# Performance work log

Measured on AMD Instinct MI355X. Metric: run time of the kernel, lower is better.

## Reference

```python
import math
import jax, jax.numpy as jnp
import numpy as np

PE_DIM = 128
NUM_HEADS = 8
U = V = 2
TEMP = 10000.0


def sine_pe(y_embed, x_embed, num_pos_feats, temperature, card):
    """Matches get_sine_position_encoding with use_norm=True."""
    eps = 1e-6
    scale = 2.0 * math.pi
    y = y_embed / (card[0] + eps) * scale
    x = x_embed / (card[1] + eps) * scale
    dim_t = jnp.asarray(temperature, jnp.float32) ** (
        2.0 * (jnp.arange(num_pos_feats, dtype=jnp.float32) // 2) / num_pos_feats)
    px = x[..., None] / dim_t
    py = y[..., None] / dim_t

    def interleave(p):
        s = jnp.sin(p[..., 0::2])
        c = jnp.cos(p[..., 1::2])
        return jnp.stack((s, c), axis=-1).reshape(p.shape[:-1] + (-1,))

    return jnp.concatenate((interleave(py), interleave(px)), axis=-1)


def setup_inputs() -> dict:
    key = jax.random.key(0)
    ks = jax.random.split(key, 8)
    B, C, H, W = 2, 64, 256, 256
    dim = C
    # xavier-ish scale for Linear(128 -> 64)
    w_std = math.sqrt(2.0 / (PE_DIM + dim))
    return {
        "feat_supp": jax.random.normal(ks[0], (B, C, H, W), jnp.float32),
        "flow": jax.random.normal(ks[1], (B, H, W, 2), jnp.float32) * 3.0,
        "feat_curr": jax.random.normal(ks[2], (B, C, H, W), jnp.float32),
        "q_w": jax.random.normal(ks[3], (dim, PE_DIM), jnp.float32) * w_std,
        "q_b": jnp.zeros((dim,), jnp.float32),
        "k_w": jax.random.normal(ks[4], (dim, PE_DIM), jnp.float32) * w_std,
        "k_b": jnp.zeros((dim,), jnp.float32),
        "v_w": jax.random.normal(ks[5], (dim, PE_DIM), jnp.float32) * w_std,
        "v_b": jnp.zeros((dim,), jnp.float32),
    }


def reference(feat_supp, flow, feat_curr, q_w, q_b, k_w, k_b, v_w, v_b):
    B, C, H, W = feat_curr.shape
    UV = U * V
    HW = H * W
    nh = NUM_HEADS
    hd = C // nh
    d = PE_DIM // C  # pe channels per feature channel
    scale = hd ** (-0.5)

    # flow-displaced integer grid + fractional part
    img_off = jnp.stack(
        jnp.meshgrid(jnp.arange(H), jnp.arange(W), indexing="ij"), axis=-1
    ).astype(flow.dtype)                                   # (H, W, 2) in (y, x)
    grid_full = img_off[None] + flow[..., ::-1]            # flow flipped to (y, x)
    grid_intg = jnp.floor(grid_full).astype(jnp.int32)
    grid_deci = grid_full - grid_intg                      # (B, H, W, 2)

    win_off = jnp.stack(
        jnp.meshgrid(jnp.arange(U), jnp.arange(V), indexing="ij"), axis=-1
    ).astype(jnp.int32)                                    # (U, V, 2)
    grid_w = grid_intg[:, :, :, None, None, :] + win_off[None, None, None]
    grid_w = grid_w.reshape(B, HW * UV, 2)
    deci = grid_deci.reshape(B, HW, 2)

    # duplicate-padding gather of support features
    h_idx = jnp.clip(grid_w[..., 0], 0, H - 1)
    w_idx = jnp.clip(grid_w[..., 1], 0, W - 1)
    lin = h_idx * W + w_idx                                # (B, HW*UV)
    feat_warp = jnp.take_along_axis(
        feat_supp.reshape(B, C, HW), lin[:, None, :], axis=2)  # (B, C, HW*UV)
    feat_warp = feat_warp.transpose(0, 2, 1).reshape(B, HW, UV, C)

    # window position bias (card = window_size - 1, use_corrected_card=False)
    wy, wx = jnp.meshgrid(jnp.arange(U, dtype=jnp.float32),
                          jnp.arange(V, dtype=jnp.float32), indexing="ij")
    pos_bias = sine_pe(wy.reshape(1, -1), wx.reshape(1, -1),
                       PE_DIM // 2, TEMP, (U - 1, V - 1))   # (1, UV, PE_DIM)
    pe_warp = pos_bias.reshape(1, 1, UV, C, d)
    fw = (feat_warp[..., None] + pe_warp).reshape(B, HW, UV, PE_DIM)

    # current-frame features + fractional-offset positional encoding
    fc = feat_curr.reshape(B, C, HW).transpose(0, 2, 1)     # (B, HW, C)
    pe_curr = sine_pe(deci[..., 0], deci[..., 1],
                      PE_DIM // 2, TEMP, (U, V))            # (B, HW, PE_DIM)
    fc = (fc[..., None] + pe_curr.reshape(B, HW, C, d)).reshape(B, HW, PE_DIM)

    q = (fc @ q_w.T + q_b).reshape(B, HW, nh, hd)
    k = (fw @ k_w.T + k_b).reshape(B, HW, UV, nh, hd)
    v = (fw @ v_w.T + v_b).reshape(B, HW, UV, nh, hd)

    attn = jnp.einsum("bnhd,bnuhd->bnhu", q * scale, k)
    attn = jax.nn.softmax(attn, axis=-1)
    out = jnp.einsum("bnhu,bnuhd->bnhd", attn, v).reshape(B, HW, C)
    return out.reshape(B, H, W, C).transpose(0, 3, 1, 2)
```

## Files before the change

### kernel.cpp

```cpp
#include <hip/hip_runtime.h>
#include <hip/hip_bf16.h>

#define HWHW 65536
#define LN1E4_32 0.28782313662425572f
#define TWO_PI_N 6.2831847f

typedef __attribute__((ext_vector_type(8))) short short8;
typedef __attribute__((ext_vector_type(4))) short s16x4;
typedef __attribute__((ext_vector_type(4))) float f32x4;


__device__ __forceinline__ short f2bf(float f) {
  union { __hip_bfloat16 h; short s; } u;
  u.h = __float2bfloat16(f);
  return u.s;
}

__global__ __launch_bounds__(256)
void pre_pass(const float* __restrict__ supp,
              const float* __restrict__ qw, const float* __restrict__ kw,
              const float* __restrict__ vw,
              const float* __restrict__ kb, const float* __restrict__ vb,
              __hip_bfloat16* __restrict__ suppT,
              __hip_bfloat16* __restrict__ wfrag, float* __restrict__ bias) {
  const int t = threadIdx.x;
  if (blockIdx.x < 2048) {
    __shared__ short tile[64 * 68];
    const int b   = blockIdx.x >> 10;
    const int p0  = (blockIdx.x & 1023) << 6;
    const int px4 = (t & 15) << 2;
    const int g   = t >> 4;

    const float* src = supp + ((size_t)b * 64 + g * 4) * HWHW + p0 + px4;
    f32x4 v[4];
#pragma unroll
    for (int c = 0; c < 4; ++c)
      v[c] = *(const f32x4*)(src + (size_t)c * HWHW);
#pragma unroll
    for (int j = 0; j < 4; ++j) {
      s16x4 pk;
#pragma unroll
      for (int c = 0; c < 4; ++c) pk[c] = f2bf(v[c][j]);
      *(s16x4*)&tile[(px4 + j) * 68 + g * 4] = pk;
    }
    __syncthreads();
    const int px = t >> 2, ch0 = (t & 3) << 4;
    s16x4 r0 = *(s16x4*)&tile[px * 68 + ch0];
    s16x4 r1 = *(s16x4*)&tile[px * 68 + ch0 + 4];
    s16x4 r2 = *(s16x4*)&tile[px * 68 + ch0 + 8];
    s16x4 r3 = *(s16x4*)&tile[px * 68 + ch0 + 12];
    short8 o0, o1;
#pragma unroll
    for (int j = 0; j < 4; ++j) {
      o0[j] = r0[j]; o0[j + 4] = r1[j];
      o1[j] = r2[j]; o1[j + 4] = r3[j];
    }
    short8* dst = (short8*)(suppT + ((size_t)(b * HWHW + p0 + px)) * 64 + ch0);
    dst[0] = o0;
    dst[1] = o1;
  } else if (blockIdx.x < 2056) {
    int slot = (blockIdx.x - 2048) * 256 + t;
    __hip_bfloat16* dst = wfrag + slot * 8;
    if (slot < 1024) {
      int ksnt = slot >> 6, lane = slot & 63;
      int ks = ksnt >> 2, nt = ksnt & 3;
      const float* w = qw + (nt * 16 + (lane & 15)) * 128 + ks * 32 + (lane >> 4) * 8;
#pragma unroll
      for (int j = 0; j < 8; ++j) dst[j] = __float2bfloat16(w[j]);
    } else {
      int mat = (slot >= 1536);
      int rem = slot & 511;
      int ksnt = rem >> 6, lane = rem & 63;
      int ks = ksnt >> 2, nt = ksnt & 3;
      int c0 = ks * 32 + (lane >> 4) * 8;
      const float* w = (mat ? vw : kw) + (nt * 16 + (lane & 15)) * 128;
#pragma unroll
      for (int j = 0; j < 8; ++j)
        dst[j] = __float2bfloat16(w[2 * (c0 + j)] + w[2 * (c0 + j) + 1]);
    }
  } else {
    for (int s = t; s < 512; s += 256) {
      int mat = s >> 8, uv = (s >> 6) & 3, c = s & 63;
      const float* w = (mat ? vw : kw) + c * 128;
      float acc = (mat ? vb : kb)[c];
      for (int kk = 0; kk < 128; ++kk) {
        float val = (kk < 64 ? (float)(uv >> 1) : (float)(uv & 1)) * TWO_PI_N;
        int i = kk & 63, f = i >> 1;
        float arg = val * __expf(-(float)f * LN1E4_32);
        float pe = (i & 1) ? __cosf(arg) : __sinf(arg);
        acc += pe * w[kk];
      }
      bias[s] = acc;
    }
  }
}

__global__ __attribute__((amdgpu_waves_per_eu(4, 4))) __launch_bounds__(256)
void iw_main(const __hip_bfloat16* __restrict__ suppT, const float* __restrict__ flow,
             const float* __restrict__ feat_curr,
             const short8* __restrict__ wg, const float* __restrict__ bias_g,
             const float* __restrict__ q_b, float* __restrict__ out)
{
  __shared__ __align__(16) char smem[35072];
  short8* lds_kv   = (short8*)smem;
  f32x4*  lds_bias = (f32x4*)(smem + 16384);
  short8* lds_qw   = (short8*)(smem + 18432);
  float*  outstage = (float*)(smem + 18432);

  const int tid = threadIdx.x;
  const int idx = ((blockIdx.x & 7) << 8) | (blockIdx.x >> 3);
  const int b   = idx >> 10;
  const int hw0 = (idx & 1023) << 6;
  const int lane = tid & 63, wv = tid >> 6;
  const int quad = lane >> 4, l15 = lane & 15;
  const int uvl  = l15 & 3;
  const int prow = l15 >> 2;
  const short8* sT = (const short8*)suppT;

#pragma unroll
  for (int j = 0; j < 4; ++j) {
    lds_qw[j * 256 + tid] = wg[j * 256 + tid];
    lds_kv[j * 256 + tid] = wg[1024 + j * 256 + tid];
  }
  {
    float* bl = (float*)lds_bias;
#pragma unroll
    for (int s_ = 0; s_ < 2; ++s_) {
      int s = s_ * 256 + tid;
      int mat = s >> 8, rem = s & 255, r = rem >> 6, c = rem & 63;
      bl[mat * 256 + (c >> 4) * 64 + (c & 15) * 4 + r] = bias_g[s];
    }
  }
  __syncthreads();

  float invd[2][4];
#pragma unroll
  for (int a = 0; a < 2; ++a)
#pragma unroll
    for (int jj = 0; jj < 4; ++jj)
      invd[a][jj] = __expf(-(float)(a * 16 + quad * 4 + jj) * LN1E4_32);

  int iy, ix;
  f32x4 qacc[4];

  {
    const int qpix = hw0 + wv * 16 + l15;
    float2 fl = ((const float2*)flow)[b * HWHW + qpix];
    float gy = (float)(qpix >> 8) + fl.y;
    float gx = (float)(qpix & 255) + fl.x;
    float fy = floorf(gy), fx = floorf(gx);
    iy = (int)fy; ix = (int)fx;
    float vy = (gy - fy) * (6.2831853071795864f / 2.000001f);
    float vx = (gx - fx) * (6.2831853071795864f / 2.000001f);

    short8 qa[4];
#pragma unroll
    for (int ks = 0; ks < 4; ++ks) {
      float val = (ks < 2) ? vy : vx;
#pragma unroll
      for (int jj = 0; jj < 4; ++jj) {
        int c = ks * 16 + quad * 4 + jj;
        float feat = feat_curr[(b * 64 + c) * HWHW + qpix];
        float arg = val * invd[ks & 1][jj];
        qa[ks][jj * 2]     = f2bf(feat + __sinf(arg));
        qa[ks][jj * 2 + 1] = f2bf(feat + __cosf(arg));
      }
    }
#pragma unroll
    for (int nt = 0; nt < 4; ++nt) qacc[nt] = (f32x4){0.f, 0.f, 0.f, 0.f};
#pragma unroll
    for (int ks = 0; ks < 4; ++ks)
#pragma unroll
      for (int nt = 0; nt < 4; ++nt)
        qacc[nt] = __builtin_amdgcn_mfma_f32_16x16x32_bf16(
            qa[ks], lds_qw[(ks * 4 + nt) * 64 + lane], qacc[nt], 0, 0, 0);
  }

  int off[4];
#pragma unroll
  for (int m = 0; m < 4; ++m) {
    int p  = m * 4 + prow;
    int yy = min(max(__shfl(iy, p) + (uvl >> 1), 0), 255);
    int xx = min(max(__shfl(ix, p) + (uvl & 1), 0), 255);
    off[m] = (b * HWHW + yy * 256 + xx) * 8;
  }

  __syncthreads();

  short8 ka[4][2];
#pragma unroll
  for (int m = 0; m < 4; ++m) {
    ka[m][0] = sT[off[m] + quad];
    ka[m][1] = sT[off[m] + 4 + quad];
  }

  float qT[4][4];
  {
#pragma unroll
    for (int nt = 0; nt < 4; ++nt) {
      float qb = q_b[nt * 16 + l15];
#pragma unroll
      for (int r = 0; r < 4; ++r)
        qacc[nt][r] = (qacc[nt][r] + qb) * 0.35355339059327373f;
    }
#pragma unroll
    for (int mt = 0; mt < 4; ++mt)
#pragma unroll
      for (int nt = 0; nt < 4; ++nt) {
        int src = mt * 16 + l15;
        float v0 = __shfl(qacc[nt][0], src);
        float v1 = __shfl(qacc[nt][1], src);
        float v2 = __shfl(qacc[nt][2], src);
        float v3 = __shfl(qacc[nt][3], src);
        float t0 = (quad & 2) ? v2 : v0;
        float t1 = (quad & 2) ? v3 : v1;
        qT[mt][nt] = (quad & 1) ? t1 : t0;
      }
  }

#pragma unroll
  for (int nt = 0; nt < 4; ++nt) {
    short8 kf0 = lds_kv[nt * 64 + lane];
    short8 kf1 = lds_kv[(4 + nt) * 64 + lane];
    short8 vf0 = lds_kv[(8 + nt) * 64 + lane];
    short8 vf1 = lds_kv[(12 + nt) * 64 + lane];
    f32x4 kb4 = lds_bias[nt * 16 + l15];
    f32x4 vb4 = lds_bias[64 + nt * 16 + l15];

#pragma unroll
    for (int mt = 0; mt < 4; ++mt) {
      f32x4 kacc = kb4;
      f32x4 vacc = vb4;
      kacc = __builtin_amdgcn_mfma_f32_16x16x32_bf16(ka[mt][0], kf0, kacc, 0, 0, 0);
      kacc = __builtin_amdgcn_mfma_f32_16x16x32_bf16(ka[mt][1], kf1, kacc, 0, 0, 0);
      vacc = __builtin_amdgcn_mfma_f32_16x16x32_bf16(ka[mt][0], vf0, vacc, 0, 0, 0);
      vacc = __builtin_amdgcn_mfma_f32_16x16x32_bf16(ka[mt][1], vf1, vacc, 0, 0, 0);

      float lg[4];
#pragma unroll
      for (int r = 0; r < 4; ++r) {
        float p = qT[mt][nt] * kacc[r];
        p += __shfl_xor(p, 1);
        p += __shfl_xor(p, 2);
        p += __shfl_xor(p, 4);
        lg[r] = p;
      }
      float mx = fmaxf(fmaxf(lg[0], lg[1]), fmaxf(lg[2], lg[3]));
      float e0 = __expf(lg[0] - mx), e1 = __expf(lg[1] - mx);
      float e2 = __expf(lg[2] - mx), e3 = __expf(lg[3] - mx);
      float inv = 1.0f / (e0 + e1 + e2 + e3);
      float o = (e0 * vacc[0] + e1 * vacc[1] + e2 * vacc[2] + e3 * vacc[3]) * inv;
      outstage[(nt * 16 + l15) * 65 + wv * 16 + mt * 4 + quad] = o;
    }
  }

  __syncthreads();
#pragma unroll
  for (int i = 0; i < 16; ++i) {
    int j = i * 256 + tid;
    int c = j >> 6, p = j & 63;
    out[(b * 64 + c) * HWHW + hw0 + p] = outstage[c * 65 + p];
  }
}

extern "C" void kernel_launch(void* const* d_in, const int* in_sizes, int n_in,
                              void* d_out, int out_size, void* d_ws, size_t ws_size,
                              hipStream_t stream) {
  const float* feat_supp = (const float*)d_in[0];
  const float* flow      = (const float*)d_in[1];
  const float* feat_curr = (const float*)d_in[2];
  const float* q_w = (const float*)d_in[3];
  const float* q_b = (const float*)d_in[4];
  const float* k_w = (const float*)d_in[5];
  const float* k_b = (const float*)d_in[6];
  const float* v_w = (const float*)d_in[7];
  const float* v_b = (const float*)d_in[8];
  float* out = (float*)d_out;
  (void)in_sizes; (void)n_in; (void)out_size; (void)ws_size;

  __hip_bfloat16* wfrag = (__hip_bfloat16*)d_ws;
  float* bias           = (float*)((char*)d_ws + 32768);
  __hip_bfloat16* suppT = (__hip_bfloat16*)((char*)d_ws + 65536);

  hipLaunchKernelGGL(pre_pass, dim3(2057), dim3(256), 0, stream,
                     feat_supp, q_w, k_w, v_w, k_b, v_b, suppT, wfrag, bias);
  hipLaunchKernelGGL(iw_main, dim3(2048), dim3(256), 0, stream,
                     suppT, flow, feat_curr, (const short8*)d_ws, bias, q_b, out);
}
```

Baseline: 153.1 us.

## Read weights from global instead of LDS, raise occupancy, use DPP reductions

The per-block copy of the Q/K/V weight fragments into shared memory is removed. The fragments are now read straight from global memory, with a double-buffered register prefetch for the Q projection. This shrinks LDS from about 35 KB to about 18.7 KB, drops one block barrier, and relaxes the waves-per-EU hint from 4 to 5–8 so more blocks can be resident to hide gather latency. The three shuffle-xor reductions are replaced with DPP quad-perm and half-mirror moves. In exchange, every wave issues repeated cached global loads for the weights, and the tighter register budget could cause spills.

Result: slower. 159.2 us (+4.0%).

```diff
diff --git a/kernel.cpp b/kernel.cpp
--- a/kernel.cpp
+++ b/kernel.cpp
@@ -95,17 +95,15 @@
   }
 }
 
-__global__ __attribute__((amdgpu_waves_per_eu(4, 4))) __launch_bounds__(256)
+__global__ __attribute__((amdgpu_waves_per_eu(5, 8))) __launch_bounds__(256)
 void iw_main(const __hip_bfloat16* __restrict__ suppT, const float* __restrict__ flow,
              const float* __restrict__ feat_curr,
              const short8* __restrict__ wg, const float* __restrict__ bias_g,
              const float* __restrict__ q_b, float* __restrict__ out)
 {
-  __shared__ __align__(16) char smem[35072];
-  short8* lds_kv   = (short8*)smem;
-  f32x4*  lds_bias = (f32x4*)(smem + 16384);
-  short8* lds_qw   = (short8*)(smem + 18432);
-  float*  outstage = (float*)(smem + 18432);
+  __shared__ __align__(16) char smem[18688];
+  f32x4* lds_bias = (f32x4*)smem;
+  float* outstage = (float*)(smem + 2048);
 
   const int tid = threadIdx.x;
   const int idx = ((blockIdx.x & 7) << 8) | (blockIdx.x >> 3);
@@ -117,11 +115,6 @@
   const int prow = l15 >> 2;
   const short8* sT = (const short8*)suppT;
 
-#pragma unroll
-  for (int j = 0; j < 4; ++j) {
-    lds_qw[j * 256 + tid] = wg[j * 256 + tid];
-    lds_kv[j * 256 + tid] = wg[1024 + j * 256 + tid];
-  }
   {
     float* bl = (float*)lds_bias;
 #pragma unroll
@@ -168,12 +161,23 @@
     }
 #pragma unroll
     for (int nt = 0; nt < 4; ++nt) qacc[nt] = (f32x4){0.f, 0.f, 0.f, 0.f};
-#pragma unroll
-    for (int ks = 0; ks < 4; ++ks)
+
+    short8 qw0[4], qw1[4];
+#pragma unroll
+    for (int i = 0; i < 4; ++i) qw0[i] = wg[i * 64 + lane];
+#pragma unroll
+    for (int ks = 0; ks < 4; ++ks) {
+      if (ks < 3) {
+        short8* dstw = (ks & 1) ? qw0 : qw1;
+#pragma unroll
+        for (int i = 0; i < 4; ++i) dstw[i] = wg[((ks + 1) * 4 + i) * 64 + lane];
+      }
+      const short8* qw = (ks & 1) ? qw1 : qw0;
 #pragma unroll
       for (int nt = 0; nt < 4; ++nt)
         qacc[nt] = __builtin_amdgcn_mfma_f32_16x16x32_bf16(
-            qa[ks], lds_qw[(ks * 4 + nt) * 64 + lane], qacc[nt], 0, 0, 0);
+            qa[ks], qw[nt], qacc[nt], 0, 0, 0);
+    }
   }
 
   int off[4];
@@ -184,8 +188,6 @@
     int xx = min(max(__shfl(ix, p) + (uvl & 1), 0), 255);
     off[m] = (b * HWHW + yy * 256 + xx) * 8;
   }
-
-  __syncthreads();
 
   short8 ka[4][2];
 #pragma unroll
@@ -220,10 +222,10 @@
 
 #pragma unroll
   for (int nt = 0; nt < 4; ++nt) {
-    short8 kf0 = lds_kv[nt * 64 + lane];
-    short8 kf1 = lds_kv[(4 + nt) * 64 + lane];
-    short8 vf0 = lds_kv[(8 + nt) * 64 + lane];
-    short8 vf1 = lds_kv[(12 + nt) * 64 + lane];
+    short8 kf0 = wg[1024 + nt * 64 + lane];
+    short8 kf1 = wg[1024 + (4 + nt) * 64 + lane];
+    short8 vf0 = wg[1024 + (8 + nt) * 64 + lane];
+    short8 vf1 = wg[1024 + (12 + nt) * 64 + lane];
     f32x4 kb4 = lds_bias[nt * 16 + l15];
     f32x4 vb4 = lds_bias[64 + nt * 16 + l15];
 
@@ -240,9 +242,12 @@
 #pragma unroll
       for (int r = 0; r < 4; ++r) {
         float p = qT[mt][nt] * kacc[r];
-        p += __shfl_xor(p, 1);
-        p += __shfl_xor(p, 2);
-        p += __shfl_xor(p, 4);
+        p += __int_as_float(__builtin_amdgcn_update_dpp(
+                 0, __float_as_int(p), 0xB1, 0xf, 0xf, true));
+        p += __int_as_float(__builtin_amdgcn_update_dpp(
+                 0, __float_as_int(p), 0x4E, 0xf, 0xf, true));
+        p += __int_as_float(__builtin_amdgcn_update_dpp(
+                 0, __float_as_int(p), 0x141, 0xf, 0xf, true));
         lg[r] = p;
       }
       float mx = fmaxf(fmaxf(lg[0], lg[1]), fmaxf(lg[2], lg[3]));
```
